# Kernel tuning notes

Measured on AMD Instinct MI355X. Metric: run time of the kernel, lower is better.

## Reference

```python
import jax, jax.numpy as jnp
import numpy as np

VOCAB = 500_000
EMB = 300
TAGS = 2

def setup_inputs() -> dict:
    key = jax.random.key(0)
    k1, k2, k3, k4, k5 = jax.random.split(key, 5)
    x = jax.random.randint(k1, (4096, 200), 0, VOCAB)  # [B, S] token ids
    emb = jax.random.normal(k2, (VOCAB, EMB), dtype=jnp.float32) * 0.05
    # nn.Linear(in, out, bias=False).weight has shape [out, in]; forward is x @ W.T
    w1 = jax.random.normal(k3, (EMB, EMB), dtype=jnp.float32) * (1.0 / np.sqrt(EMB))
    w2 = jax.random.normal(k4, (EMB, EMB), dtype=jnp.float32) * (1.0 / np.sqrt(EMB))
    w3 = jax.random.normal(k5, (TAGS, EMB), dtype=jnp.float32) * (1.0 / np.sqrt(EMB))
    return {"x": x, "emb": emb, "w1": w1, "w2": w2, "w3": w3}

def reference(x, emb, w1, w2, w3):
    # fused gather + mean pool (replaces the per-token Python loop)
    pooled = jnp.mean(emb[x], axis=1)            # [B, EMB]
    h = jax.nn.relu(pooled @ w1.T)               # [B, EMB]
    h = jax.nn.relu(h @ w2.T)                    # [B, EMB]
    return h @ w3.T                              # [B, TAGS]
```

## Files before the change

kernel.cpp:

```cpp
#include <hip/hip_runtime.h>
#include <hip/hip_bf16.h>

#define B_SZ   4096
#define S_LEN  200
#define EMB    300
#define TAGS   2

__global__ __launch_bounds__(256)
void gather_mean_kernel(const int* __restrict__ x,
                        const float* __restrict__ emb,
                        float* __restrict__ pooled) {
    const int b   = blockIdx.x;
    const int tid = threadIdx.x;

    __shared__ int ids[S_LEN];
    if (tid < S_LEN) ids[tid] = x[b * S_LEN + tid];
    __syncthreads();

    const int  d0   = tid;
    const int  d1   = tid + 256;
    const bool has2 = (d1 < EMB);

    float acc0 = 0.f, acc1 = 0.f;
#pragma unroll 8
    for (int t = 0; t < S_LEN; ++t) {
        const long base = (long)ids[t] * EMB;
        acc0 += emb[base + d0];
        if (has2) acc1 += emb[base + d1];
    }
    const float inv = 1.0f / (float)S_LEN;
    pooled[(long)b * EMB + d0] = acc0 * inv;
    if (has2) pooled[(long)b * EMB + d1] = acc1 * inv;
}

#define BM 64
#define BN 64
#define BK 16

template <bool RELU>
__global__ __launch_bounds__(256)
void gemm_tn_kernel(const float* __restrict__ A,
                    const float* __restrict__ W,
                    float* __restrict__ C,
                    int M, int N, int K) {
    __shared__ float As[BM][BK + 1];
    __shared__ float Ws[BN][BK + 1];

    const int tid = threadIdx.x;
    const int tx  = tid % 16;
    const int ty  = tid / 16;
    const int m0  = blockIdx.x * BM;
    const int n0  = blockIdx.y * BN;

    float acc[4][4] = {};

    for (int k0 = 0; k0 < K; k0 += BK) {
        {
            const int r  = tid / 4;
            const int c  = (tid % 4) * 4;
            const int gk = k0 + c;
            float4 v = make_float4(0.f, 0.f, 0.f, 0.f);
            const long off = (long)(m0 + r) * K + gk;
            if (gk + 3 < K) {
                v = *(const float4*)&A[off];
            } else {
                float t0 = (gk + 0 < K) ? A[off + 0] : 0.f;
                float t1 = (gk + 1 < K) ? A[off + 1] : 0.f;
                float t2 = (gk + 2 < K) ? A[off + 2] : 0.f;
                float t3 = (gk + 3 < K) ? A[off + 3] : 0.f;
                v = make_float4(t0, t1, t2, t3);
            }
            As[r][c + 0] = v.x; As[r][c + 1] = v.y;
            As[r][c + 2] = v.z; As[r][c + 3] = v.w;
        }
        {
            const int r  = tid / 4;
            const int c  = (tid % 4) * 4;
            const int gn = n0 + r;
            const int gk = k0 + c;
            float4 v = make_float4(0.f, 0.f, 0.f, 0.f);
            if (gn < N) {
                const long off = (long)gn * K + gk;
                if (gk + 3 < K) {
                    v = *(const float4*)&W[off];
                } else {
                    float t0 = (gk + 0 < K) ? W[off + 0] : 0.f;
                    float t1 = (gk + 1 < K) ? W[off + 1] : 0.f;
                    float t2 = (gk + 2 < K) ? W[off + 2] : 0.f;
                    float t3 = (gk + 3 < K) ? W[off + 3] : 0.f;
                    v = make_float4(t0, t1, t2, t3);
                }
            }
            Ws[r][c + 0] = v.x; Ws[r][c + 1] = v.y;
            Ws[r][c + 2] = v.z; Ws[r][c + 3] = v.w;
        }
        __syncthreads();

#pragma unroll
        for (int kk = 0; kk < BK; ++kk) {
            float a[4], bb[4];
#pragma unroll
            for (int i = 0; i < 4; ++i) a[i]  = As[ty * 4 + i][kk];
#pragma unroll
            for (int j = 0; j < 4; ++j) bb[j] = Ws[tx * 4 + j][kk];
#pragma unroll
            for (int i = 0; i < 4; ++i)
#pragma unroll
                for (int j = 0; j < 4; ++j)
                    acc[i][j] = fmaf(a[i], bb[j], acc[i][j]);
        }
        __syncthreads();
    }

#pragma unroll
    for (int i = 0; i < 4; ++i) {
        const int gm = m0 + ty * 4 + i;
#pragma unroll
        for (int j = 0; j < 4; ++j) {
            const int gn = n0 + tx * 4 + j;
            if (gn < N) {
                float v = acc[i][j];
                if (RELU) v = fmaxf(v, 0.f);
                C[(long)gm * N + gn] = v;
            }
        }
    }
}

__global__ __launch_bounds__(256)
void final_kernel(const float* __restrict__ H,
                  const float* __restrict__ w3,
                  float* __restrict__ out) {
    const int wave = threadIdx.x >> 6;
    const int lane = threadIdx.x & 63;
    const int row  = blockIdx.x * 4 + wave;
    if (row >= B_SZ) return;

    float a0 = 0.f, a1 = 0.f;
    for (int k = lane; k < EMB; k += 64) {
        const float h = H[(long)row * EMB + k];
        a0 += h * w3[k];
        a1 += h * w3[EMB + k];
    }
#pragma unroll
    for (int off = 32; off > 0; off >>= 1) {
        a0 += __shfl_down(a0, off);
        a1 += __shfl_down(a1, off);
    }
    if (lane == 0) {
        out[row * TAGS + 0] = a0;
        out[row * TAGS + 1] = a1;
    }
}

extern "C" void kernel_launch(void* const* d_in, const int* in_sizes, int n_in,
                              void* d_out, int out_size, void* d_ws, size_t ws_size,
                              hipStream_t stream) {
    const int*   x   = (const int*)d_in[0];
    const float* emb = (const float*)d_in[1];
    const float* w1  = (const float*)d_in[2];
    const float* w2  = (const float*)d_in[3];
    const float* w3  = (const float*)d_in[4];
    float*       out = (float*)d_out;

    float* pooled = (float*)d_ws;
    float* h1     = pooled + (long)B_SZ * EMB;

    gather_mean_kernel<<<B_SZ, 256, 0, stream>>>(x, emb, pooled);

    dim3 gemm_grid(B_SZ / BM, (EMB + BN - 1) / BN);
    gemm_tn_kernel<true><<<gemm_grid, 256, 0, stream>>>(pooled, w1, h1, B_SZ, EMB, EMB);
    gemm_tn_kernel<true><<<gemm_grid, 256, 0, stream>>>(h1, w2, pooled, B_SZ, EMB, EMB);

    final_kernel<<<(B_SZ + 3) / 4, 256, 0, stream>>>(pooled, w3, out);
}
```

Measured before the change: 932.9 us.

## Vectorize embedding gather across waves and restructure GEMM tiles to 512 threads

The gather kernel now assigns each wave a subset of tokens and reads each embedding row with float4 loads, then reduces the four per-wave partial sums through shared memory. This replaces scalar per-dimension loads with wider ones and spreads tokens across waves. The GEMM kernel moves to 512 threads with transposed (k-major) shared tiles, vectorized LDS reads and a 4x2 per-thread micro-tile, splitting staging of A and W across thread halves. The float4 embedding loads depend on 16-byte alignment of each row, which holds because EMB is 300, a multiple of 4. The extra shared-memory reduction and the smaller per-thread tile add some overhead.

```diff
diff --git a/kernel.cpp b/kernel.cpp
--- a/kernel.cpp
+++ b/kernel.cpp
@@ -10,104 +10,114 @@
 void gather_mean_kernel(const int* __restrict__ x,
                         const float* __restrict__ emb,
                         float* __restrict__ pooled) {
-    const int b   = blockIdx.x;
-    const int tid = threadIdx.x;
+    const int b    = blockIdx.x;
+    const int tid  = threadIdx.x;
+    const int wave = tid >> 6;
+    const int lane = tid & 63;
 
-    __shared__ int ids[S_LEN];
+    __shared__ int   ids[S_LEN];
+    __shared__ float part[4][EMB + 4];
+
     if (tid < S_LEN) ids[tid] = x[b * S_LEN + tid];
     __syncthreads();
 
-    const int  d0   = tid;
-    const int  d1   = tid + 256;
-    const bool has2 = (d1 < EMB);
+    float4 acc0 = make_float4(0.f, 0.f, 0.f, 0.f);
+    float4 acc1 = make_float4(0.f, 0.f, 0.f, 0.f);
+    const bool has2 = (lane < (EMB - 256 + 3) / 4);
 
-    float acc0 = 0.f, acc1 = 0.f;
-#pragma unroll 8
-    for (int t = 0; t < S_LEN; ++t) {
+#pragma unroll 2
+    for (int i = 0; i < S_LEN / 4; ++i) {
+        const int  t    = wave + 4 * i;
         const long base = (long)ids[t] * EMB;
-        acc0 += emb[base + d0];
-        if (has2) acc1 += emb[base + d1];
+        const float4 v0 = *(const float4*)&emb[base + 4 * lane];
+        acc0.x += v0.x; acc0.y += v0.y; acc0.z += v0.z; acc0.w += v0.w;
+        if (has2) {
+            const float4 v1 = *(const float4*)&emb[base + 256 + 4 * lane];
+            acc1.x += v1.x; acc1.y += v1.y; acc1.z += v1.z; acc1.w += v1.w;
+        }
     }
+
+    *(float4*)&part[wave][4 * lane] = acc0;
+    if (has2) *(float4*)&part[wave][256 + 4 * lane] = acc1;
+    __syncthreads();
+
     const float inv = 1.0f / (float)S_LEN;
-    pooled[(long)b * EMB + d0] = acc0 * inv;
-    if (has2) pooled[(long)b * EMB + d1] = acc1 * inv;
+    {
+        const float s = part[0][tid] + part[1][tid] + part[2][tid] + part[3][tid];
+        pooled[(long)b * EMB + tid] = s * inv;
+    }
+    if (tid < EMB - 256) {
+        const int d = 256 + tid;
+        const float s = part[0][d] + part[1][d] + part[2][d] + part[3][d];
+        pooled[(long)b * EMB + d] = s * inv;
+    }
 }
 
-#define BM 64
-#define BN 64
-#define BK 16
+#define BM   64
+#define BN   64
+#define BK   16
+#define LDST 68
 
 template <bool RELU>
-__global__ __launch_bounds__(256)
+__global__ __launch_bounds__(512)
 void gemm_tn_kernel(const float* __restrict__ A,
                     const float* __restrict__ W,
                     float* __restrict__ C,
                     int M, int N, int K) {
-    __shared__ float As[BM][BK + 1];
-    __shared__ float Ws[BN][BK + 1];
+    __shared__ float As[BK][LDST];
+    __shared__ float Ws[BK][LDST];
 
     const int tid = threadIdx.x;
-    const int tx  = tid % 16;
-    const int ty  = tid / 16;
+    const int tx  = tid & 31;
+    const int ty  = tid >> 5;
     const int m0  = blockIdx.x * BM;
     const int n0  = blockIdx.y * BN;
 
-    float acc[4][4] = {};
+    const bool stageA = (tid < 256);
+    const int  s  = stageA ? tid : tid - 256;
+    const int  sr = s >> 2;
+    const int  sc = (s & 3) * 4;
+
+    float acc[4][2] = {};
 
     for (int k0 = 0; k0 < K; k0 += BK) {
         {
-            const int r  = tid / 4;
-            const int c  = (tid % 4) * 4;
-            const int gk = k0 + c;
+            const int    gk   = k0 + sc;
+            const float* src  = stageA ? A : W;
+            const int    grow = stageA ? (m0 + sr) : (n0 + sr);
             float4 v = make_float4(0.f, 0.f, 0.f, 0.f);
-            const long off = (long)(m0 + r) * K + gk;
-            if (gk + 3 < K) {
-                v = *(const float4*)&A[off];
-            } else {
-                float t0 = (gk + 0 < K) ? A[off + 0] : 0.f;
-                float t1 = (gk + 1 < K) ? A[off + 1] : 0.f;
-                float t2 = (gk + 2 < K) ? A[off + 2] : 0.f;
-                float t3 = (gk + 3 < K) ? A[off + 3] : 0.f;
-                v = make_float4(t0, t1, t2, t3);
-            }
-            As[r][c + 0] = v.x; As[r][c + 1] = v.y;
-            As[r][c + 2] = v.z; As[r][c + 3] = v.w;
-        }
-        {
-            const int r  = tid / 4;
-            const int c  = (tid % 4) * 4;
-            const int gn = n0 + r;
-            const int gk = k0 + c;
-            float4 v = make_float4(0.f, 0.f, 0.f, 0.f);
-            if (gn < N) {
-                const long off = (long)gn * K + gk;
+            const bool rowok = stageA ? true : (grow < N);
+            if (rowok) {
+                const long off = (long)grow * K + gk;
                 if (gk + 3 < K) {
-                    v = *(const float4*)&W[off];
+                    v = *(const float4*)&src[off];
                 } else {
-                    float t0 = (gk + 0 < K) ? W[off + 0] : 0.f;
-                    float t1 = (gk + 1 < K) ? W[off + 1] : 0.f;
-                    float t2 = (gk + 2 < K) ? W[off + 2] : 0.f;
-                    float t3 = (gk + 3 < K) ? W[off + 3] : 0.f;
-                    v = make_float4(t0, t1, t2, t3);
+                    if (gk + 0 < K) v.x = src[off + 0];
+                    if (gk + 1 < K) v.y = src[off + 1];
+                    if (gk + 2 < K) v.z = src[off + 2];
+                    if (gk + 3 < K) v.w = src[off + 3];
                 }
             }
-            Ws[r][c + 0] = v.x; Ws[r][c + 1] = v.y;
-            Ws[r][c + 2] = v.z; Ws[r][c + 3] = v.w;
+            float (*dst)[LDST] = stageA ? As : Ws;
+            dst[sc + 0][sr] = v.x;
+            dst[sc + 1][sr] = v.y;
+            dst[sc + 2][sr] = v.z;
+            dst[sc + 3][sr] = v.w;
         }
         __syncthreads();
 
 #pragma unroll
         for (int kk = 0; kk < BK; ++kk) {
-            float a[4], bb[4];
-#pragma unroll
-            for (int i = 0; i < 4; ++i) a[i]  = As[ty * 4 + i][kk];
-#pragma unroll
-            for (int j = 0; j < 4; ++j) bb[j] = Ws[tx * 4 + j][kk];
-#pragma unroll
-            for (int i = 0; i < 4; ++i)
-#pragma unroll
-                for (int j = 0; j < 4; ++j)
-                    acc[i][j] = fmaf(a[i], bb[j], acc[i][j]);
+            const float4 a  = *(const float4*)&As[kk][ty * 4];
+            const float2 bb = *(const float2*)&Ws[kk][tx * 2];
+            acc[0][0] = fmaf(a.x, bb.x, acc[0][0]);
+            acc[0][1] = fmaf(a.x, bb.y, acc[0][1]);
+            acc[1][0] = fmaf(a.y, bb.x, acc[1][0]);
+            acc[1][1] = fmaf(a.y, bb.y, acc[1][1]);
+            acc[2][0] = fmaf(a.z, bb.x, acc[2][0]);
+            acc[2][1] = fmaf(a.z, bb.y, acc[2][1]);
+            acc[3][0] = fmaf(a.w, bb.x, acc[3][0]);
+            acc[3][1] = fmaf(a.w, bb.y, acc[3][1]);
         }
         __syncthreads();
     }
@@ -116,8 +126,8 @@
     for (int i = 0; i < 4; ++i) {
         const int gm = m0 + ty * 4 + i;
 #pragma unroll
-        for (int j = 0; j < 4; ++j) {
-            const int gn = n0 + tx * 4 + j;
+        for (int j = 0; j < 2; ++j) {
+            const int gn = n0 + tx * 2 + j;
             if (gn < N) {
                 float v = acc[i][j];
                 if (RELU) v = fmaxf(v, 0.f);
@@ -169,8 +179,8 @@
     gather_mean_kernel<<<B_SZ, 256, 0, stream>>>(x, emb, pooled);
 
     dim3 gemm_grid(B_SZ / BM, (EMB + BN - 1) / BN);
-    gemm_tn_kernel<true><<<gemm_grid, 256, 0, stream>>>(pooled, w1, h1, B_SZ, EMB, EMB);
-    gemm_tn_kernel<true><<<gemm_grid, 256, 0, stream>>>(h1, w2, pooled, B_SZ, EMB, EMB);
+    gemm_tn_kernel<true><<<gemm_grid, 512, 0, stream>>>(pooled, w1, h1, B_SZ, EMB, EMB);
+    gemm_tn_kernel<true><<<gemm_grid, 512, 0, stream>>>(h1, w2, pooled, B_SZ, EMB, EMB);
 
     final_kernel<<<(B_SZ + 3) / 4, 256, 0, stream>>>(pooled, w3, out);
 }
```

Measured after the change: 829.7 us. 1.12x faster.
